# Kernel optimization log

Measured on AMD Instinct MI355X. Metric: run time of the kernel, lower is better.

Reference implementation:

```python
import jax, jax.numpy as jnp
import numpy as np

B, L, H, V = 16, 512, 256, 32000
HALF = H // 2
EPS_LN = 1e-5
EPS_NORM = 1e-12


def setup_inputs() -> dict:
    key = jax.random.key(0)
    ks = jax.random.split(key, 9)
    s = 0.02
    return {
        "seq": jax.random.randint(ks[0], (B, L), 0, V),
        "embed": jax.random.normal(ks[1], (V, H), jnp.float32) * s,
        "W1": jax.random.normal(ks[2], (2 * H, H), jnp.float32) * s,
        "b1": jnp.zeros((2 * H,), jnp.float32),
        "W2": jax.random.normal(ks[3], (H, 2 * H), jnp.float32) * s,
        "b2": jnp.zeros((H,), jnp.float32),
        "gamma": jnp.ones((H,), jnp.float32),
        "beta": jnp.zeros((H,), jnp.float32),
        "W_sem": jax.random.normal(ks[4], (HALF, H), jnp.float32) * s,
        "W_epi": jax.random.normal(ks[5], (HALF, H), jnp.float32) * s,
        "W_rp": jax.random.normal(ks[6], (H, H), jnp.float32) * s,
        "b_rp": jnp.zeros((H,), jnp.float32),
        "W_out": jax.random.normal(ks[7], (V, H), jnp.float32) * s,
        "b_out": jnp.zeros((V,), jnp.float32),
    }


def _l2norm(x):
    # F.normalize(dim=-1): x / max(||x||, eps)
    n = jnp.sqrt(jnp.sum(x * x, axis=-1, keepdims=True))
    return x / jnp.maximum(n, EPS_NORM)


def reference(seq, embed, W1, b1, W2, b2, gamma, beta, W_sem, W_epi, W_rp, b_rp, W_out, b_out):
    h = embed[seq]                                   # [B, L, H]
    ff = jnp.maximum(h @ W1.T + b1, 0.0) @ W2.T + b2  # MLP with 2H hidden
    x = h + ff
    mu = jnp.mean(x, axis=-1, keepdims=True)
    var = jnp.var(x, axis=-1, keepdims=True)
    h = (x - mu) / jnp.sqrt(var + EPS_LN) * gamma + beta  # LayerNorm

    ks_all = jnp.einsum('blh,kh->blk', h, W_sem)     # [B, L, HALF]
    ke_all = jnp.einsum('blh,kh->blk', h, W_epi)

    def step(carry, kv):
        M_s, M_e = carry
        k_s, k_e = kv                                 # [B, HALF] each
        kns = _l2norm(k_s)
        kne = _l2norm(k_e)
        vps = jnp.einsum('bij,bj->bi', M_s, kns)      # read from fast weights
        vpe = jnp.einsum('bij,bj->bi', M_e, kne)
        M_s = M_s + jnp.einsum('bi,bj->bij', k_s - vps, kns)  # delta-rule write
        M_e = M_e + jnp.einsum('bi,bj->bij', k_e - vpe, kne)
        return (M_s, M_e), None

    M0 = jnp.zeros((B, HALF, HALF), h.dtype)
    # scan over timesteps 0..L-2 (time-major)
    (M_s, M_e), _ = jax.lax.scan(
        step, (M0, M0),
        (jnp.swapaxes(ks_all[:, :-1], 0, 1), jnp.swapaxes(ke_all[:, :-1], 0, 1)))

    cs = jnp.einsum('bij,bj->bi', M_s, ks_all[:, -1])  # read with last-token query
    ce = jnp.einsum('bij,bj->bi', M_e, ke_all[:, -1])
    c = jnp.concatenate([cs, ce], axis=-1)             # [B, H]
    r = c @ W_rp.T + b_rp
    return r @ W_out.T + b_out                          # [B, V]
```

## Files before the change

kernel.cpp:

```cpp
#include <hip/hip_runtime.h>

#define B_ 16
#define L_ 512
#define H_ 256
#define V_ 32000
#define HALF_ 128

typedef __attribute__((ext_vector_type(8))) short short8;
typedef __attribute__((ext_vector_type(4))) float floatx4;
typedef __attribute__((ext_vector_type(2))) float float2v;

__device__ __forceinline__ unsigned short f2bf(float x) {
  unsigned int u = __float_as_uint(x);
  unsigned int r = (u + 0x7FFFu + ((u >> 16) & 1u)) >> 16;
  return (unsigned short)r;
}

template <int CTRL>
__device__ __forceinline__ float dpp_xor_add(float x) {
  int y = __builtin_amdgcn_mov_dpp(__float_as_int(x), CTRL, 0xf, 0xf, true);
  return x + __int_as_float(y);
}

__device__ __forceinline__ float redu16(float p) {
  p = dpp_xor_add<0xB1>(p);
  p = dpp_xor_add<0x4E>(p);
  p = dpp_xor_add<0x141>(p);
  p = dpp_xor_add<0x140>(p);
  return p;
}

__device__ __forceinline__ float2v pk_fma(float2v a, float2v b, float2v c) {
  float2v d;
  asm("v_pk_fma_f32 %0, %1, %2, %3" : "=v"(d) : "v"(a), "v"(b), "v"(c));
  return d;
}
__device__ __forceinline__ float2v pk_mul(float2v a, float2v b) {
  float2v d;
  asm("v_pk_mul_f32 %0, %1, %2" : "=v"(d) : "v"(a), "v"(b));
  return d;
}

__device__ __forceinline__ void async_cp16(const float* g, float* l) {
  __builtin_amdgcn_global_load_lds(
      (const __attribute__((address_space(1))) void*)g,
      (__attribute__((address_space(3))) void*)l, 16, 0, 0);
}

__device__ __forceinline__ uint4 load8cvt(const float* p) {
  float4 a = ((const float4*)p)[0];
  float4 b = ((const float4*)p)[1];
  uint4 r;
  r.x = (unsigned)f2bf(a.x) | ((unsigned)f2bf(a.y) << 16);
  r.y = (unsigned)f2bf(a.z) | ((unsigned)f2bf(a.w) << 16);
  r.z = (unsigned)f2bf(b.x) | ((unsigned)f2bf(b.y) << 16);
  r.w = (unsigned)f2bf(b.z) | ((unsigned)f2bf(b.w) << 16);
  return r;
}

__global__ __launch_bounds__(256) void prep_kernel(const float* __restrict__ W1,
                                                   const float* __restrict__ W2,
                                                   const float* __restrict__ Ws,
                                                   const float* __restrict__ We,
                                                   unsigned short* __restrict__ W1b,
                                                   unsigned short* __restrict__ W2b,
                                                   unsigned short* __restrict__ Wcb) {
  int i = blockIdx.x * 256 + threadIdx.x;
  if (i < 131072) W1b[i] = f2bf(W1[i]);
  else if (i < 262144) W2b[i - 131072] = f2bf(W2[i - 131072]);
  else if (i < 294912) Wcb[i - 262144] = f2bf(Ws[i - 262144]);
  else Wcb[i - 262144] = f2bf(We[i - 294912]);
}

__global__ __launch_bounds__(256) void gemm1_kernel(const int* __restrict__ seq,
                                                    const float* __restrict__ embed,
                                                    const unsigned short* __restrict__ W1b,
                                                    const float* __restrict__ b1,
                                                    unsigned short* __restrict__ a1b) {
  __shared__ unsigned short As[128 * 40];
  __shared__ unsigned short Bs[128 * 40];
  int tid = threadIdx.x;
  int wave = tid >> 6, lane = tid & 63;
  int wm = (wave >> 1) * 64, wn = (wave & 1) * 64;
  int quad = lane >> 4, l15 = lane & 15;
  int bm = blockIdx.y * 128, bn = blockIdx.x * 128;
  int sr = tid >> 2, sq = tid & 3;

  int tok0 = seq[bm + sr];
  int tok1 = seq[bm + 64 + sr];

  floatx4 zero = {0.f, 0.f, 0.f, 0.f};
  floatx4 acc[4][4];
#pragma unroll
  for (int fi = 0; fi < 4; fi++)
#pragma unroll
    for (int fj = 0; fj < 4; fj++) acc[fi][fj] = zero;

  uint4 av0 = load8cvt(embed + (size_t)tok0 * H_ + sq * 8);
  uint4 av1 = load8cvt(embed + (size_t)tok1 * H_ + sq * 8);
  uint4 bv0 = *(const uint4*)(W1b + (size_t)(bn + sr) * 256 + sq * 8);
  uint4 bv1 = *(const uint4*)(W1b + (size_t)(bn + 64 + sr) * 256 + sq * 8);

  for (int k0 = 0; k0 < 256; k0 += 32) {
    __syncthreads();
    *(uint4*)(As + sr * 40 + sq * 8) = av0;
    *(uint4*)(As + (64 + sr) * 40 + sq * 8) = av1;
    *(uint4*)(Bs + sr * 40 + sq * 8) = bv0;
    *(uint4*)(Bs + (64 + sr) * 40 + sq * 8) = bv1;
    __syncthreads();
    if (k0 + 32 < 256) {
      av0 = load8cvt(embed + (size_t)tok0 * H_ + k0 + 32 + sq * 8);
      av1 = load8cvt(embed + (size_t)tok1 * H_ + k0 + 32 + sq * 8);
      bv0 = *(const uint4*)(W1b + (size_t)(bn + sr) * 256 + k0 + 32 + sq * 8);
      bv1 = *(const uint4*)(W1b + (size_t)(bn + 64 + sr) * 256 + k0 + 32 + sq * 8);
    }
    short8 af[4], bf[4];
#pragma unroll
    for (int f = 0; f < 4; f++) {
      af[f] = *(const short8*)(As + (wm + f * 16 + l15) * 40 + quad * 8);
      bf[f] = *(const short8*)(Bs + (wn + f * 16 + l15) * 40 + quad * 8);
    }
#pragma unroll
    for (int fi = 0; fi < 4; fi++)
#pragma unroll
      for (int fj = 0; fj < 4; fj++)
        acc[fi][fj] = __builtin_amdgcn_mfma_f32_16x16x32_bf16(af[fi], bf[fj], acc[fi][fj], 0, 0, 0);
  }

#pragma unroll
  for (int fi = 0; fi < 4; fi++) {
#pragma unroll
    for (int fj = 0; fj < 4; fj++) {
      int col = bn + wn + fj * 16 + l15;
      float bb = b1[col];
#pragma unroll
      for (int rg = 0; rg < 4; rg++) {
        int row = bm + wm + fi * 16 + quad * 4 + rg;
        float v = fmaxf(acc[fi][fj][rg] + bb, 0.f);
        a1b[(size_t)row * 512 + col] = f2bf(v);
      }
    }
  }
}

__global__ __launch_bounds__(256) void mlpk_kernel(const unsigned short* __restrict__ a1b,
                                                   const unsigned short* __restrict__ W2b,
                                                   const float* __restrict__ b2,
                                                   const int* __restrict__ seq,
                                                   const float* __restrict__ embed,
                                                   const float* __restrict__ gamma,
                                                   const float* __restrict__ beta,
                                                   const unsigned short* __restrict__ Wcb,
                                                   float* __restrict__ khat,
                                                   float* __restrict__ nrm) {
  __shared__ unsigned short As[32 * 40];
  __shared__ unsigned short Bs[256 * 40];
  __shared__ unsigned short hnS[32 * 264];
  __shared__ float stats[2][2][32];
  __shared__ float stg[2][32 * 132];
  int tid = threadIdx.x;
  int wave = tid >> 6, lane = tid & 63;
  int wm = (wave >> 1) * 16, wnh = wave & 1, wn = wnh * 128;
  int quad = lane >> 4, l15 = lane & 15;
  int bm = blockIdx.x * 32;
  int sr = tid >> 2, sq = tid & 3;

  floatx4 zero = {0.f, 0.f, 0.f, 0.f};
  floatx4 acc[8];
#pragma unroll
  for (int fj = 0; fj < 8; fj++) acc[fj] = zero;

  uint4 av, bv[4];
  if (tid < 128) av = *(const uint4*)(a1b + (size_t)(bm + sr) * 512 + sq * 8);
#pragma unroll
  for (int q = 0; q < 4; q++) {
    int unit = q * 256 + tid;
    bv[q] = *(const uint4*)(W2b + (size_t)(unit >> 2) * 512 + (unit & 3) * 8);
  }
  for (int k0 = 0; k0 < 512; k0 += 32) {
    __syncthreads();
    if (tid < 128) *(uint4*)(As + sr * 40 + sq * 8) = av;
#pragma unroll
    for (int q = 0; q < 4; q++) {
      int unit = q * 256 + tid;
      *(uint4*)(Bs + (unit >> 2) * 40 + (unit & 3) * 8) = bv[q];
    }
    __syncthreads();
    if (k0 + 32 < 512) {
      if (tid < 128) av = *(const uint4*)(a1b + (size_t)(bm + sr) * 512 + k0 + 32 + sq * 8);
#pragma unroll
      for (int q = 0; q < 4; q++) {
        int unit = q * 256 + tid;
        bv[q] = *(const uint4*)(W2b + (size_t)(unit >> 2) * 512 + k0 + 32 + (unit & 3) * 8);
      }
    }
    short8 af = *(const short8*)(As + (wm + l15) * 40 + quad * 8);
    short8 bf[8];
#pragma unroll
    for (int fj = 0; fj < 8; fj++)
      bf[fj] = *(const short8*)(Bs + (wn + fj * 16 + l15) * 40 + quad * 8);
#pragma unroll
    for (int fj = 0; fj < 8; fj++)
      acc[fj] = __builtin_amdgcn_mfma_f32_16x16x32_bf16(af, bf[fj], acc[fj], 0, 0, 0);
  }

  int seqv[4];
#pragma unroll
  for (int rg = 0; rg < 4; rg++) seqv[rg] = seq[bm + wm + quad * 4 + rg];
  float v[8][4];
#pragma unroll
  for (int fj = 0; fj < 8; fj++) {
    int col = wn + fj * 16 + l15;
    float bb = b2[col];
#pragma unroll
    for (int rg = 0; rg < 4; rg++)
      v[fj][rg] = acc[fj][rg] + bb + embed[(size_t)seqv[rg] * H_ + col];
  }
  float s_[4], q_[4];
#pragma unroll
  for (int rg = 0; rg < 4; rg++) {
    float s = 0.f, q = 0.f;
#pragma unroll
    for (int fj = 0; fj < 8; fj++) {
      s += v[fj][rg];
      q += v[fj][rg] * v[fj][rg];
    }
    s_[rg] = redu16(s);
    q_[rg] = redu16(q);
  }
  if (l15 == 0) {
#pragma unroll
    for (int rg = 0; rg < 4; rg++) {
      int rlocal = wm + quad * 4 + rg;
      stats[wnh][0][rlocal] = s_[rg];
      stats[wnh][1][rlocal] = q_[rg];
    }
  }
  __syncthreads();
#pragma unroll
  for (int rg = 0; rg < 4; rg++) {
    int rlocal = wm + quad * 4 + rg;
    float sum = stats[0][0][rlocal] + stats[1][0][rlocal];
    float ssq = stats[0][1][rlocal] + stats[1][1][rlocal];
    float mu = sum * (1.f / H_);
    float var = ssq * (1.f / H_) - mu * mu;
    float inv = rsqrtf(var + 1e-5f);
#pragma unroll
    for (int fj = 0; fj < 8; fj++) {
      int col = wn + fj * 16 + l15;
      float y = (v[fj][rg] - mu) * inv * gamma[col] + beta[col];
      hnS[rlocal * 264 + col] = f2bf(y);
    }
  }
  __syncthreads();

  floatx4 acc2[8];
#pragma unroll
  for (int fj = 0; fj < 8; fj++) acc2[fj] = zero;
#pragma unroll
  for (int q = 0; q < 4; q++) {
    int unit = q * 256 + tid;
    bv[q] = *(const uint4*)(Wcb + (size_t)(unit >> 2) * 256 + (unit & 3) * 8);
  }
  for (int k0 = 0; k0 < 256; k0 += 32) {
    __syncthreads();
#pragma unroll
    for (int q = 0; q < 4; q++) {
      int unit = q * 256 + tid;
      *(uint4*)(Bs + (unit >> 2) * 40 + (unit & 3) * 8) = bv[q];
    }
    __syncthreads();
    if (k0 + 32 < 256) {
#pragma unroll
      for (int q = 0; q < 4; q++) {
        int unit = q * 256 + tid;
        bv[q] = *(const uint4*)(Wcb + (size_t)(unit >> 2) * 256 + k0 + 32 + (unit & 3) * 8);
      }
    }
    short8 af = *(const short8*)(hnS + (wm + l15) * 264 + k0 + quad * 8);
    short8 bf[8];
#pragma unroll
    for (int fj = 0; fj < 8; fj++)
      bf[fj] = *(const short8*)(Bs + (wn + fj * 16 + l15) * 40 + quad * 8);
#pragma unroll
    for (int fj = 0; fj < 8; fj++)
      acc2[fj] = __builtin_amdgcn_mfma_f32_16x16x32_bf16(af, bf[fj], acc2[fj], 0, 0, 0);
  }

  int b = bm >> 9;
  int idxm = b * 2 + wnh;
  int tloc0 = (bm & 511) + wm + quad * 4;
  float inv[4], nr4[4];
#pragma unroll
  for (int rg = 0; rg < 4; rg++) {
    float ssq = 0.f;
#pragma unroll
    for (int fj = 0; fj < 8; fj++) ssq += acc2[fj][rg] * acc2[fj][rg];
    ssq = redu16(ssq);
    nr4[rg] = fmaxf(sqrtf(ssq), 1e-12f);
    inv[rg] = 1.f / nr4[rg];
  }
  if (l15 == 0) {
#pragma unroll
    for (int rg = 0; rg < 4; rg++) nrm[(size_t)idxm * L_ + tloc0 + rg] = nr4[rg];
  }
#pragma unroll
  for (int fj = 0; fj < 8; fj++) {
    int ch = fj * 16 + l15;
    int j = ch >> 2, e = ch & 3;
    int pj = (j & 1) ? (16 + (j >> 1)) : (j >> 1);
    int pcol = pj * 4 + e;
    int trl = wm + quad * 4;
#pragma unroll
    for (int rg = 0; rg < 4; rg++)
      stg[wnh][(trl + rg) * 132 + pcol] = acc2[fj][rg] * inv[rg];
  }
  __syncthreads();
#pragma unroll
  for (int f = 0; f < 8; f++) {
    int idx = f * 256 + tid;
    int w = idx >> 10, rem = idx & 1023;
    int tr = rem >> 5, l = rem & 31;
    float4 vv = *(float4*)&stg[w][tr * 132 + l * 4];
    int im = (bm >> 9) * 2 + w;
    *(float4*)&khat[((size_t)im * L_ + (bm & 511) + tr) * HALF_ + l * 4] = vv;
  }
}

#define STEP(KP, KH, NR)                                                 \
  do {                                                                   \
    float2v t_ = pk_mul(m01, KP[0]);                                     \
    t_ = pk_fma(m23, KP[1], t_);                                         \
    t_ = pk_fma(m45, KP[2], t_);                                         \
    t_ = pk_fma(m67, KP[3], t_);                                         \
    float p_ = t_.x + t_.y;                                              \
    p_ = redu16(p_);                                                     \
    float sv_ = (KH) * (NR)-p_;                                          \
    float2v s2_ = {sv_, sv_};                                            \
    m01 = pk_fma(s2_, KP[0], m01);                                       \
    m23 = pk_fma(s2_, KP[1], m23);                                       \
    m45 = pk_fma(s2_, KP[2], m45);                                       \
    m67 = pk_fma(s2_, KP[3], m67);                                       \
  } while (0)

#define LOADPK(DST, PTR)                                                 \
  do {                                                                   \
    float4 a_ = *(const float4*)(PTR);                                   \
    float4 b_ = *(const float4*)((PTR) + 64);                            \
    DST[0] = (float2v){a_.x, a_.y};                                      \
    DST[1] = (float2v){a_.z, a_.w};                                      \
    DST[2] = (float2v){b_.x, b_.y};                                      \
    DST[3] = (float2v){b_.z, b_.w};                                      \
  } while (0)

__global__ __launch_bounds__(256) void scan_kernel(const float* __restrict__ khat,
                                                   const float* __restrict__ nrm,
                                                   float* __restrict__ c) {
  __shared__ float sk[2][64 * 128];
  int bid = blockIdx.x;
  int idxm = bid & 31;
  int rg = bid >> 5;
  int b = idxm >> 1, mat = idxm & 1;
  const float* kh = khat + (size_t)idxm * L_ * HALF_;
  const float* np = nrm + (size_t)idxm * L_;

  int tid = threadIdx.x;
  int wave = tid >> 6, lane = tid & 63;
  int seg = tid & 15, rl = tid >> 4;
  int r = rg * 16 + rl;
  int jj = r >> 2, ee = r & 3;
  int pj = (jj & 1) ? (16 + (jj >> 1)) : (jj >> 1);
  int prow = pj * 4 + ee;

  float2v m01 = {0.f, 0.f}, m23 = {0.f, 0.f}, m45 = {0.f, 0.f}, m67 = {0.f, 0.f};

#pragma unroll
  for (int j = 0; j < 8; j++)
    async_cp16(kh + wave * 2048 + j * 256 + lane * 4, &sk[0][wave * 2048 + j * 256] + lane * 4);
  __syncthreads();

  float4 nrn = *(const float4*)(np);
  const float* lb = &sk[0][0] + seg * 4;
  const float* lk = &sk[0][0] + prow;

  for (int ch = 0; ch < 7; ch++) {
#pragma unroll
    for (int j = 0; j < 8; j++)
      async_cp16(kh + (size_t)(ch + 1) * 8192 + wave * 2048 + j * 256 + lane * 4,
                 &sk[(ch + 1) & 1][wave * 2048 + j * 256] + lane * 4);
    const float* base = lb + (ch & 1) * 8192;
    const float* kb2 = lk + (ch & 1) * 8192;
    float2v pk[4][4];
    float kh4[4];
#pragma unroll
    for (int u = 0; u < 4; u++) {
      LOADPK(pk[u], base + u * 128);
      kh4[u] = kb2[u * 128];
    }
    for (int g = 0; g < 15; g++) {
      float4 nrc = nrn;
      nrn = *(const float4*)(np + ch * 64 + g * 4 + 4);
#pragma unroll
      for (int u = 0; u < 4; u++) {
        STEP(pk[u], kh4[u], ((u == 0) ? nrc.x : (u == 1) ? nrc.y : (u == 2) ? nrc.z : nrc.w));
        int tn = g * 4 + u + 4;
        LOADPK(pk[u], base + tn * 128);
        kh4[u] = kb2[tn * 128];
      }
    }
    {
      float4 nrc = nrn;
      nrn = *(const float4*)(np + ch * 64 + 64);
      STEP(pk[0], kh4[0], nrc.x);
      STEP(pk[1], kh4[1], nrc.y);
      STEP(pk[2], kh4[2], nrc.z);
      STEP(pk[3], kh4[3], nrc.w);
    }
    __syncthreads();
  }

  {
    const float* base = lb + 8192;
    const float* kb2 = lk + 8192;
    float2v pk[4][4];
    float kh4[4];
#pragma unroll
    for (int u = 0; u < 4; u++) {
      LOADPK(pk[u], base + u * 128);
      kh4[u] = kb2[u * 128];
    }
    for (int g = 0; g < 15; g++) {
      float4 nrc = nrn;
      nrn = *(const float4*)(np + 448 + g * 4 + 4);
#pragma unroll
      for (int u = 0; u < 4; u++) {
        STEP(pk[u], kh4[u], ((u == 0) ? nrc.x : (u == 1) ? nrc.y : (u == 2) ? nrc.z : nrc.w));
        int tn = g * 4 + u + 4;
        LOADPK(pk[u], base + tn * 128);
        kh4[u] = kb2[tn * 128];
      }
    }
    float4 nrc = nrn;
    STEP(pk[0], kh4[0], nrc.x);
    STEP(pk[1], kh4[1], nrc.y);
    STEP(pk[2], kh4[2], nrc.z);
    float2v tq = pk_mul(m01, pk[3][0]);
    tq = pk_fma(m23, pk[3][1], tq);
    tq = pk_fma(m45, pk[3][2], tq);
    tq = pk_fma(m67, pk[3][3], tq);
    float p = redu16(tq.x + tq.y) * nrc.w;
    if (seg == 0) c[(size_t)b * H_ + mat * HALF_ + r] = p;
  }
}

__global__ void rp_kernel(const float* __restrict__ c, const float* __restrict__ Wrp,
                          const float* __restrict__ brp, float* __restrict__ r) {
  int b = blockIdx.x;
  int n = threadIdx.x;
  __shared__ float cs[H_];
  cs[n] = c[(size_t)b * H_ + n];
  __syncthreads();
  const float4* w4 = (const float4*)(Wrp + (size_t)n * H_);
  const float4* c4 = (const float4*)cs;
  float acc = 0.f;
#pragma unroll 8
  for (int k = 0; k < H_ / 4; k++) {
    float4 w = w4[k], cc = c4[k];
    acc += w.x * cc.x + w.y * cc.y + w.z * cc.z + w.w * cc.w;
  }
  r[(size_t)b * H_ + n] = acc + brp[n];
}

__global__ __launch_bounds__(256) void out_kernel(const float* __restrict__ r,
                                                  const float* __restrict__ Wout,
                                                  const float* __restrict__ bout,
                                                  float* __restrict__ out) {
  __shared__ float rs[16 * 272];
  __shared__ float obuf[16 * 68];
  int tid = threadIdx.x;
#pragma unroll
  for (int q = 0; q < 16; q++) {
    int idx = q * 256 + tid;
    int bb = idx >> 8, cc = idx & 255;
    rs[bb * 272 + cc + 4 * (cc >> 6)] = r[idx];
  }
  __syncthreads();
  int row = tid >> 2, part = tid & 3;
  int v = blockIdx.x * 64 + row;
  const float4* w4 = (const float4*)(Wout + (size_t)v * H_ + part * 64);
  float acc[16];
#pragma unroll
  for (int bb = 0; bb < 16; bb++) acc[bb] = 0.f;
#pragma unroll 4
  for (int j = 0; j < 16; j++) {
    float4 w = w4[j];
#pragma unroll
    for (int bb = 0; bb < 16; bb++) {
      float4 rv = *(const float4*)&rs[bb * 272 + part * 68 + j * 4];
      acc[bb] += w.x * rv.x + w.y * rv.y + w.z * rv.z + w.w * rv.w;
    }
  }
  float bo = bout[v];
#pragma unroll
  for (int bb = 0; bb < 16; bb++) {
    acc[bb] = dpp_xor_add<0xB1>(acc[bb]);
    acc[bb] = dpp_xor_add<0x4E>(acc[bb]);
  }
#pragma unroll
  for (int q = 0; q < 4; q++) {
    int bb = part * 4 + q;
    obuf[bb * 68 + row] = acc[bb] + bo;
  }
  __syncthreads();
#pragma unroll
  for (int q = 0; q < 4; q++) {
    int idx = q * 256 + tid;
    int bb = idx >> 6, vl = idx & 63;
    out[(size_t)bb * V_ + blockIdx.x * 64 + vl] = obuf[bb * 68 + vl];
  }
}

extern "C" void kernel_launch(void* const* d_in, const int* in_sizes, int n_in,
                              void* d_out, int out_size, void* d_ws, size_t ws_size,
                              hipStream_t stream) {
  const int* seq = (const int*)d_in[0];
  const float* embed = (const float*)d_in[1];
  const float* W1 = (const float*)d_in[2];
  const float* b1 = (const float*)d_in[3];
  const float* W2 = (const float*)d_in[4];
  const float* b2 = (const float*)d_in[5];
  const float* gamma = (const float*)d_in[6];
  const float* beta = (const float*)d_in[7];
  const float* Wsem = (const float*)d_in[8];
  const float* Wepi = (const float*)d_in[9];
  const float* Wrp = (const float*)d_in[10];
  const float* brp = (const float*)d_in[11];
  const float* Wout = (const float*)d_in[12];
  const float* bout = (const float*)d_in[13];
  float* out = (float*)d_out;

  float* ws = (float*)d_ws;
  unsigned short* a1b = (unsigned short*)ws;
  float* khat = ws + 2097152;
  float* nrm = ws + 4194304;
  unsigned short* W1b = (unsigned short*)(ws + 4210688);
  unsigned short* W2b = (unsigned short*)(ws + 4276224);
  unsigned short* Wcb = (unsigned short*)(ws + 4341760);
  float* c = ws + 4374528;
  float* r = ws + 4378624;

  prep_kernel<<<1280, 256, 0, stream>>>(W1, W2, Wsem, Wepi, W1b, W2b, Wcb);
  gemm1_kernel<<<dim3(4, 64), 256, 0, stream>>>(seq, embed, W1b, b1, a1b);
  mlpk_kernel<<<256, 256, 0, stream>>>(a1b, W2b, b2, seq, embed, gamma, beta, Wcb, khat, nrm);
  scan_kernel<<<256, 256, 0, stream>>>(khat, nrm, c);
  rp_kernel<<<16, 256, 0, stream>>>(c, Wrp, brp, r);
  out_kernel<<<500, 256, 0, stream>>>(r, Wout, bout, out);
}
```

Before: 231.6 us.

## Fold weight conversion into gemm1 and give each scan thread two matrix rows

```diff
diff --git a/kernel.cpp b/kernel.cpp
--- a/kernel.cpp
+++ b/kernel.cpp
@@ -58,32 +58,44 @@
   return r;
 }
 
-__global__ __launch_bounds__(256) void prep_kernel(const float* __restrict__ W1,
-                                                   const float* __restrict__ W2,
-                                                   const float* __restrict__ Ws,
-                                                   const float* __restrict__ We,
-                                                   unsigned short* __restrict__ W1b,
-                                                   unsigned short* __restrict__ W2b,
-                                                   unsigned short* __restrict__ Wcb) {
-  int i = blockIdx.x * 256 + threadIdx.x;
-  if (i < 131072) W1b[i] = f2bf(W1[i]);
-  else if (i < 262144) W2b[i - 131072] = f2bf(W2[i - 131072]);
-  else if (i < 294912) Wcb[i - 262144] = f2bf(Ws[i - 262144]);
-  else Wcb[i - 262144] = f2bf(We[i - 294912]);
-}
-
 __global__ __launch_bounds__(256) void gemm1_kernel(const int* __restrict__ seq,
                                                     const float* __restrict__ embed,
-                                                    const unsigned short* __restrict__ W1b,
+                                                    const float* __restrict__ W1,
                                                     const float* __restrict__ b1,
-                                                    unsigned short* __restrict__ a1b) {
+                                                    const float* __restrict__ W2,
+                                                    const float* __restrict__ Ws,
+                                                    const float* __restrict__ We,
+                                                    unsigned short* __restrict__ a1b,
+                                                    unsigned short* __restrict__ W2b,
+                                                    unsigned short* __restrict__ Wcb) {
   __shared__ unsigned short As[128 * 40];
   __shared__ unsigned short Bs[128 * 40];
+  int blk = blockIdx.x;
   int tid = threadIdx.x;
+
+  if (blk >= 256) {
+    int base = (blk - 256) * 1024 + tid * 4;
+    const float* src;
+    unsigned short* dst;
+    if (base < 131072) {
+      src = W2 + base;
+      dst = W2b + base;
+    } else {
+      int o = base - 131072;
+      src = (o < 32768) ? (Ws + o) : (We + (o - 32768));
+      dst = Wcb + o;
+    }
+    float4 v = *(const float4*)src;
+    ushort4 o4;
+    o4.x = f2bf(v.x); o4.y = f2bf(v.y); o4.z = f2bf(v.z); o4.w = f2bf(v.w);
+    *(ushort4*)dst = o4;
+    return;
+  }
+
   int wave = tid >> 6, lane = tid & 63;
   int wm = (wave >> 1) * 64, wn = (wave & 1) * 64;
   int quad = lane >> 4, l15 = lane & 15;
-  int bm = blockIdx.y * 128, bn = blockIdx.x * 128;
+  int bm = (blk >> 2) * 128, bn = (blk & 3) * 128;
   int sr = tid >> 2, sq = tid & 3;
 
   int tok0 = seq[bm + sr];
@@ -98,8 +110,8 @@
 
   uint4 av0 = load8cvt(embed + (size_t)tok0 * H_ + sq * 8);
   uint4 av1 = load8cvt(embed + (size_t)tok1 * H_ + sq * 8);
-  uint4 bv0 = *(const uint4*)(W1b + (size_t)(bn + sr) * 256 + sq * 8);
-  uint4 bv1 = *(const uint4*)(W1b + (size_t)(bn + 64 + sr) * 256 + sq * 8);
+  uint4 bv0 = load8cvt(W1 + (size_t)(bn + sr) * 256 + sq * 8);
+  uint4 bv1 = load8cvt(W1 + (size_t)(bn + 64 + sr) * 256 + sq * 8);
 
   for (int k0 = 0; k0 < 256; k0 += 32) {
     __syncthreads();
@@ -111,8 +123,8 @@
     if (k0 + 32 < 256) {
       av0 = load8cvt(embed + (size_t)tok0 * H_ + k0 + 32 + sq * 8);
       av1 = load8cvt(embed + (size_t)tok1 * H_ + k0 + 32 + sq * 8);
-      bv0 = *(const uint4*)(W1b + (size_t)(bn + sr) * 256 + k0 + 32 + sq * 8);
-      bv1 = *(const uint4*)(W1b + (size_t)(bn + 64 + sr) * 256 + k0 + 32 + sq * 8);
+      bv0 = load8cvt(W1 + (size_t)(bn + sr) * 256 + k0 + 32 + sq * 8);
+      bv1 = load8cvt(W1 + (size_t)(bn + 64 + sr) * 256 + k0 + 32 + sq * 8);
     }
     short8 af[4], bf[4];
 #pragma unroll
@@ -327,20 +339,28 @@
   }
 }
 
-#define STEP(KP, KH, NR)                                                 \
+#define STEP2(KP, KH0, KH1, NR)                                          \
   do {                                                                   \
-    float2v t_ = pk_mul(m01, KP[0]);                                     \
-    t_ = pk_fma(m23, KP[1], t_);                                         \
-    t_ = pk_fma(m45, KP[2], t_);                                         \
-    t_ = pk_fma(m67, KP[3], t_);                                         \
-    float p_ = t_.x + t_.y;                                              \
-    p_ = redu16(p_);                                                     \
-    float sv_ = (KH) * (NR)-p_;                                          \
-    float2v s2_ = {sv_, sv_};                                            \
-    m01 = pk_fma(s2_, KP[0], m01);                                       \
-    m23 = pk_fma(s2_, KP[1], m23);                                       \
-    m45 = pk_fma(s2_, KP[2], m45);                                       \
-    m67 = pk_fma(s2_, KP[3], m67);                                       \
+    float2v ta_ = pk_mul(a01, KP[0]);                                    \
+    float2v tb_ = pk_mul(b01, KP[0]);                                    \
+    ta_ = pk_fma(a23, KP[1], ta_);                                       \
+    tb_ = pk_fma(b23, KP[1], tb_);                                       \
+    ta_ = pk_fma(a45, KP[2], ta_);                                       \
+    tb_ = pk_fma(b45, KP[2], tb_);                                       \
+    ta_ = pk_fma(a67, KP[3], ta_);                                       \
+    tb_ = pk_fma(b67, KP[3], tb_);                                       \
+    float p0_ = ta_.x + ta_.y, p1_ = tb_.x + tb_.y;                      \
+    p0_ = dpp_xor_add<0xB1>(p0_);  p1_ = dpp_xor_add<0xB1>(p1_);         \
+    p0_ = dpp_xor_add<0x4E>(p0_);  p1_ = dpp_xor_add<0x4E>(p1_);         \
+    p0_ = dpp_xor_add<0x141>(p0_); p1_ = dpp_xor_add<0x141>(p1_);        \
+    p0_ = dpp_xor_add<0x140>(p0_); p1_ = dpp_xor_add<0x140>(p1_);        \
+    float s0_ = (KH0) * (NR)-p0_;                                        \
+    float s1_ = (KH1) * (NR)-p1_;                                        \
+    float2v s0v_ = {s0_, s0_}, s1v_ = {s1_, s1_};                        \
+    a01 = pk_fma(s0v_, KP[0], a01);  b01 = pk_fma(s1v_, KP[0], b01);     \
+    a23 = pk_fma(s0v_, KP[1], a23);  b23 = pk_fma(s1v_, KP[1], b23);     \
+    a45 = pk_fma(s0v_, KP[2], a45);  b45 = pk_fma(s1v_, KP[2], b45);     \
+    a67 = pk_fma(s0v_, KP[3], a67);  b67 = pk_fma(s1v_, KP[3], b67);     \
   } while (0)
 
 #define LOADPK(DST, PTR)                                                 \
@@ -353,7 +373,13 @@
     DST[3] = (float2v){b_.z, b_.w};                                      \
   } while (0)
 
-__global__ __launch_bounds__(256) void scan_kernel(const float* __restrict__ khat,
+__device__ __forceinline__ int permrow(int rr) {
+  int jj = rr >> 2, ee = rr & 3;
+  int pj = (jj & 1) ? (16 + (jj >> 1)) : (jj >> 1);
+  return pj * 4 + ee;
+}
+
+__global__ __launch_bounds__(128) void scan_kernel(const float* __restrict__ khat,
                                                    const float* __restrict__ nrm,
                                                    float* __restrict__ c) {
   __shared__ float sk[2][64 * 128];
@@ -366,90 +392,112 @@
 
   int tid = threadIdx.x;
   int wave = tid >> 6, lane = tid & 63;
-  int seg = tid & 15, rl = tid >> 4;
-  int r = rg * 16 + rl;
-  int jj = r >> 2, ee = r & 3;
-  int pj = (jj & 1) ? (16 + (jj >> 1)) : (jj >> 1);
-  int prow = pj * 4 + ee;
-
-  float2v m01 = {0.f, 0.f}, m23 = {0.f, 0.f}, m45 = {0.f, 0.f}, m67 = {0.f, 0.f};
-
-#pragma unroll
-  for (int j = 0; j < 8; j++)
-    async_cp16(kh + wave * 2048 + j * 256 + lane * 4, &sk[0][wave * 2048 + j * 256] + lane * 4);
+  int seg = tid & 15;
+  int rp_i = tid >> 4;
+  int r0 = rg * 16 + rp_i;
+  int r1 = r0 + 8;
+  int prow0 = permrow(r0), prow1 = permrow(r1);
+
+  float2v a01 = {0.f, 0.f}, a23 = {0.f, 0.f}, a45 = {0.f, 0.f}, a67 = {0.f, 0.f};
+  float2v b01 = {0.f, 0.f}, b23 = {0.f, 0.f}, b45 = {0.f, 0.f}, b67 = {0.f, 0.f};
+
+#pragma unroll
+  for (int j = 0; j < 16; j++) {
+    int slice = j * 2 + wave;
+    async_cp16(kh + slice * 256 + lane * 4, &sk[0][slice * 256] + lane * 4);
+  }
   __syncthreads();
 
   float4 nrn = *(const float4*)(np);
   const float* lb = &sk[0][0] + seg * 4;
-  const float* lk = &sk[0][0] + prow;
+  const float* lk0 = &sk[0][0] + prow0;
+  const float* lk1 = &sk[0][0] + prow1;
 
   for (int ch = 0; ch < 7; ch++) {
 #pragma unroll
-    for (int j = 0; j < 8; j++)
-      async_cp16(kh + (size_t)(ch + 1) * 8192 + wave * 2048 + j * 256 + lane * 4,
-                 &sk[(ch + 1) & 1][wave * 2048 + j * 256] + lane * 4);
+    for (int j = 0; j < 16; j++) {
+      int slice = j * 2 + wave;
+      async_cp16(kh + (size_t)(ch + 1) * 8192 + slice * 256 + lane * 4,
+                 &sk[(ch + 1) & 1][slice * 256] + lane * 4);
+    }
     const float* base = lb + (ch & 1) * 8192;
-    const float* kb2 = lk + (ch & 1) * 8192;
+    const float* ka2 = lk0 + (ch & 1) * 8192;
+    const float* kb2 = lk1 + (ch & 1) * 8192;
     float2v pk[4][4];
-    float kh4[4];
+    float kh4a[4], kh4b[4];
 #pragma unroll
     for (int u = 0; u < 4; u++) {
       LOADPK(pk[u], base + u * 128);
-      kh4[u] = kb2[u * 128];
+      kh4a[u] = ka2[u * 128];
+      kh4b[u] = kb2[u * 128];
     }
     for (int g = 0; g < 15; g++) {
       float4 nrc = nrn;
       nrn = *(const float4*)(np + ch * 64 + g * 4 + 4);
 #pragma unroll
       for (int u = 0; u < 4; u++) {
-        STEP(pk[u], kh4[u], ((u == 0) ? nrc.x : (u == 1) ? nrc.y : (u == 2) ? nrc.z : nrc.w));
+        STEP2(pk[u], kh4a[u], kh4b[u],
+              ((u == 0) ? nrc.x : (u == 1) ? nrc.y : (u == 2) ? nrc.z : nrc.w));
         int tn = g * 4 + u + 4;
         LOADPK(pk[u], base + tn * 128);
-        kh4[u] = kb2[tn * 128];
+        kh4a[u] = ka2[tn * 128];
+        kh4b[u] = kb2[tn * 128];
       }
     }
     {
       float4 nrc = nrn;
       nrn = *(const float4*)(np + ch * 64 + 64);
-      STEP(pk[0], kh4[0], nrc.x);
-      STEP(pk[1], kh4[1], nrc.y);
-      STEP(pk[2], kh4[2], nrc.z);
-      STEP(pk[3], kh4[3], nrc.w);
+      STEP2(pk[0], kh4a[0], kh4b[0], nrc.x);
+      STEP2(pk[1], kh4a[1], kh4b[1], nrc.y);
+      STEP2(pk[2], kh4a[2], kh4b[2], nrc.z);
+      STEP2(pk[3], kh4a[3], kh4b[3], nrc.w);
     }
     __syncthreads();
   }
 
   {
     const float* base = lb + 8192;
-    const float* kb2 = lk + 8192;
+    const float* ka2 = lk0 + 8192;
+    const float* kb2 = lk1 + 8192;
     float2v pk[4][4];
-    float kh4[4];
+    float kh4a[4], kh4b[4];
 #pragma unroll
     for (int u = 0; u < 4; u++) {
       LOADPK(pk[u], base + u * 128);
-      kh4[u] = kb2[u * 128];
+      kh4a[u] = ka2[u * 128];
+      kh4b[u] = kb2[u * 128];
     }
     for (int g = 0; g < 15; g++) {
       float4 nrc = nrn;
       nrn = *(const float4*)(np + 448 + g * 4 + 4);
 #pragma unroll
       for (int u = 0; u < 4; u++) {
-        STEP(pk[u], kh4[u], ((u == 0) ? nrc.x : (u == 1) ? nrc.y : (u == 2) ? nrc.z : nrc.w));
+        STEP2(pk[u], kh4a[u], kh4b[u],
+              ((u == 0) ? nrc.x : (u == 1) ? nrc.y : (u == 2) ? nrc.z : nrc.w));
         int tn = g * 4 + u + 4;
         LOADPK(pk[u], base + tn * 128);
-        kh4[u] = kb2[tn * 128];
+        kh4a[u] = ka2[tn * 128];
+        kh4b[u] = kb2[tn * 128];
       }
     }
     float4 nrc = nrn;
-    STEP(pk[0], kh4[0], nrc.x);
-    STEP(pk[1], kh4[1], nrc.y);
-    STEP(pk[2], kh4[2], nrc.z);
-    float2v tq = pk_mul(m01, pk[3][0]);
-    tq = pk_fma(m23, pk[3][1], tq);
-    tq = pk_fma(m45, pk[3][2], tq);
-    tq = pk_fma(m67, pk[3][3], tq);
-    float p = redu16(tq.x + tq.y) * nrc.w;
-    if (seg == 0) c[(size_t)b * H_ + mat * HALF_ + r] = p;
+    STEP2(pk[0], kh4a[0], kh4b[0], nrc.x);
+    STEP2(pk[1], kh4a[1], kh4b[1], nrc.y);
+    STEP2(pk[2], kh4a[2], kh4b[2], nrc.z);
+    float2v ta = pk_mul(a01, pk[3][0]);
+    float2v tb = pk_mul(b01, pk[3][0]);
+    ta = pk_fma(a23, pk[3][1], ta);
+    tb = pk_fma(b23, pk[3][1], tb);
+    ta = pk_fma(a45, pk[3][2], ta);
+    tb = pk_fma(b45, pk[3][2], tb);
+    ta = pk_fma(a67, pk[3][3], ta);
+    tb = pk_fma(b67, pk[3][3], tb);
+    float p0 = redu16(ta.x + ta.y) * nrc.w;
+    float p1 = redu16(tb.x + tb.y) * nrc.w;
+    if (seg == 0) {
+      c[(size_t)b * H_ + mat * HALF_ + r0] = p0;
+      c[(size_t)b * H_ + mat * HALF_ + r1] = p1;
+    }
   }
 }
 
@@ -543,16 +591,14 @@
   unsigned short* a1b = (unsigned short*)ws;
   float* khat = ws + 2097152;
   float* nrm = ws + 4194304;
-  unsigned short* W1b = (unsigned short*)(ws + 4210688);
-  unsigned short* W2b = (unsigned short*)(ws + 4276224);
-  unsigned short* Wcb = (unsigned short*)(ws + 4341760);
-  float* c = ws + 4374528;
-  float* r = ws + 4378624;
-
-  prep_kernel<<<1280, 256, 0, stream>>>(W1, W2, Wsem, Wepi, W1b, W2b, Wcb);
-  gemm1_kernel<<<dim3(4, 64), 256, 0, stream>>>(seq, embed, W1b, b1, a1b);
+  unsigned short* W2b = (unsigned short*)(ws + 4210688);
+  unsigned short* Wcb = (unsigned short*)(ws + 4276224);
+  float* c = ws + 4308992;
+  float* r = ws + 4313088;
+
+  gemm1_kernel<<<448, 256, 0, stream>>>(seq, embed, W1, b1, W2, Wsem, Wepi, a1b, W2b, Wcb);
   mlpk_kernel<<<256, 256, 0, stream>>>(a1b, W2b, b2, seq, embed, gamma, beta, Wcb, khat, nrm);
-  scan_kernel<<<256, 256, 0, stream>>>(khat, nrm, c);
+  scan_kernel<<<256, 128, 0, stream>>>(khat, nrm, c);
   rp_kernel<<<16, 256, 0, stream>>>(c, Wrp, brp, r);
   out_kernel<<<500, 256, 0, stream>>>(r, Wout, bout, out);
 }
```

New measurement: 236.9 us. +2.3%, slower.
